# Optimization experiments

Measured on AMD Instinct MI355X. Metric: run time of the kernel, lower is better.

## Reference

```python
import jax, jax.numpy as jnp
import numpy as np

WINDOW = 1024  # sliding-window mask_mod: attend to keys within WINDOW behind the query


def setup_inputs() -> dict:
    key = jax.random.key(0)
    B, L, H, E = 2, 2048, 16, 64
    qkv = jax.random.normal(key, (B, L, 3, H, E), dtype=jnp.float32)
    return {"qkv": qkv}


def reference(qkv) -> jnp.ndarray:
    # Training path of FlexAttention.forward (key_cache/val_cache/cache_seqlens = None).
    B, L, _, H, E = qkv.shape
    q = qkv[:, :, 0]  # [b, l, h, e]
    k = qkv[:, :, 1]
    v = qkv[:, :, 2]

    scale = 1.0 / (E ** 0.5)  # flex_attention default softmax scaling
    scores = jnp.einsum("bqhe,bkhe->bhqk", q, k) * scale  # [b, h, q, kv]

    q_idx = jnp.arange(L)[:, None]
    kv_idx = jnp.arange(L)[None, :]
    dist = q_idx - kv_idx  # [q, kv]

    # score_mod: ALiBi bias, slope_h = 2^(-8*(h+1)/H)
    slopes = jnp.exp2(-8.0 * (jnp.arange(H, dtype=jnp.float32) + 1.0) / H)
    scores = scores - slopes[None, :, None, None] * dist.astype(jnp.float32)

    # and_masks(mask_mod, causal_mask): sliding window AND causal
    mask = (dist >= 0) & (dist < WINDOW)  # causal guarantees >=1 valid key per row
    scores = jnp.where(mask[None, None], scores, -jnp.inf)

    attn = jax.nn.softmax(scores, axis=-1)
    out = jnp.einsum("bhqk,bkhe->bqhe", attn, v)  # [b, l, h, e]
    return out
```

## Files before the change

kernel.cpp:

```cpp
#include <hip/hip_runtime.h>
#include <cstdint>

#define L_SEQ 2048
#define NH 16
#define EDIM 64
#define WINDOW 1024
#define QT 64
#define KT 64
#define LOG2E 1.4426950408889634f
#define M_FIX 16.0f

typedef short bf16x8 __attribute__((ext_vector_type(8)));
typedef short bf16x4 __attribute__((ext_vector_type(4)));
typedef float f32x4 __attribute__((ext_vector_type(4)));

__device__ __forceinline__ short f2bf(float x) {
    uint32_t u = __builtin_bit_cast(uint32_t, x);
    uint32_t r = (u + 0x7fffu + ((u >> 16) & 1u)) >> 16;
    return (short)(r & 0xffffu);
}
__device__ __forceinline__ short f2bf_trunc(float x) {
    return (short)(__builtin_bit_cast(uint32_t, x) >> 16);
}

__device__ __forceinline__ f32x4 mfma16(bf16x4 a, bf16x4 b, f32x4 c) {
#if __has_builtin(__builtin_amdgcn_mfma_f32_16x16x16bf16_1k)
    return __builtin_amdgcn_mfma_f32_16x16x16bf16_1k(a, b, c, 0, 0, 0);
#else
    asm("s_nop 1\n\tv_mfma_f32_16x16x16_bf16 %0, %1, %2, %0"
        : "+v"(c) : "v"(a), "v"(b));
    return c;
#endif
}

__device__ __forceinline__ void async16(const short* g, const short* l) {
    __builtin_amdgcn_global_load_lds(
        (const __attribute__((address_space(1))) void*)(uintptr_t)(g),
        (__attribute__((address_space(3))) void*)(uintptr_t)(l),
        16, 0, 0);
}

__global__ __launch_bounds__(256) void prepass4(const float* __restrict__ qkv,
        short* __restrict__ kw, short* __restrict__ vw) {
    __shared__ float vt[64][68];
    const int x = blockIdx.x;
    const int xcd = x & 7, y = x >> 3;
    const int pairid = xcd * 4 + (y >> 5);
    const int tile = y & 31;
    const int b = pairid >> 4, h = pairid & 15;
    const int tid = threadIdx.x;
    const int tg = pairid * 32 + tile;
    const float* base = qkv + (size_t)b * (L_SEQ * 3072) + (size_t)tile * 64 * 3072 + h * 64;
    short* ko = kw + (size_t)tg * 4096;
    short* vo = vw + (size_t)tg * 4096;

    #pragma unroll
    for (int it = 0; it < 2; ++it) {
        const int c = tid + it * 256;
        const int row = c >> 3, cc = (c & 7) ^ (row & 7);
        const float* src = base + (size_t)row * 3072 + 1024 + cc * 8;
        float4 a = *(const float4*)src, d = *(const float4*)(src + 4);
        short* o = ko + (size_t)c * 8;
        o[0] = f2bf(a.x); o[1] = f2bf(a.y); o[2] = f2bf(a.z); o[3] = f2bf(a.w);
        o[4] = f2bf(d.x); o[5] = f2bf(d.y); o[6] = f2bf(d.z); o[7] = f2bf(d.w);
    }
    {
        const int row = tid >> 2, e0 = (tid & 3) << 4;
        const float* src = base + (size_t)row * 3072 + 2048 + e0;
        #pragma unroll
        for (int q4 = 0; q4 < 4; ++q4) {
            float4 a = *(const float4*)(src + q4 * 4);
            vt[e0 + q4 * 4 + 0][row] = a.x;
            vt[e0 + q4 * 4 + 1][row] = a.y;
            vt[e0 + q4 * 4 + 2][row] = a.z;
            vt[e0 + q4 * 4 + 3][row] = a.w;
        }
    }
    __syncthreads();
    #pragma unroll
    for (int it = 0; it < 2; ++it) {
        const int c = tid + it * 256;
        const int et = c >> 7, a = (c >> 6) & 1, l6 = c & 63;
        const int quad = l6 >> 4, r16 = l6 & 15;
        const int e = et * 16 + r16;
        float4 x0 = *(const float4*)&vt[e][a * 32 + quad * 4];
        float4 x1 = *(const float4*)&vt[e][a * 32 + 16 + quad * 4];
        bf16x8 o8;
        o8[0] = f2bf(x0.x); o8[1] = f2bf(x0.y); o8[2] = f2bf(x0.z); o8[3] = f2bf(x0.w);
        o8[4] = f2bf(x1.x); o8[5] = f2bf(x1.y); o8[6] = f2bf(x1.z); o8[7] = f2bf(x1.w);
        *(bf16x8*)(vo + (size_t)c * 8) = o8;
    }
}

__global__ __launch_bounds__(128, 2) void flexattn_fwd6(
        const float* __restrict__ qkv, const short* __restrict__ kw,
        const short* __restrict__ vw, float* __restrict__ out) {
    __shared__ __align__(16) short kS[2][4096];
    __shared__ __align__(16) short vS[2][4096];

    const int s = blockIdx.y & 31;
    const int k = blockIdx.y >> 5;
    const int t16 = (s + ((k >> 1) << 4)) & 31;
    const int qtile = (k & 1) ? (31 - t16) : t16;
    const int pairid = blockIdx.x * 4 + k;
    const int h = pairid & 15;
    const int b = pairid >> 4;

    const int tid  = threadIdx.x;
    const int w    = tid >> 6;
    const int lane = tid & 63;
    const int quad = lane >> 4;
    const int r16  = lane & 15;
    const int qb   = qtile * QT;
    const int bh32 = (b * NH + h) * 32;
    const int q0   = qb + w * 32 + r16;

    const int t0q = (qb >= WINDOW - 1) ? ((qb - (WINDOW - 1)) >> 6) : 0;
    const int t1  = qtile;
    const int swz = quad ^ (r16 & 7);
    const int cb0 = w * 256;

    {
        const short* ktile = kw + (size_t)(bh32 + t0q) * 4096;
        const short* vtile = vw + (size_t)(bh32 + t0q) * 4096;
        #pragma unroll
        for (int i = 0; i < 4; ++i) {
            const int cb = cb0 + i * 64;
            async16(ktile + (size_t)(cb + lane) * 8, &kS[0][cb * 8]);
            async16(vtile + (size_t)(cb + lane) * 8, &vS[0][cb * 8]);
        }
    }

    const float qscale = 0.125f * LOG2E;
    bf16x8 qfrag[2][2];
    #pragma unroll
    for (int g = 0; g < 2; ++g) {
        const float* qrow = qkv + (size_t)b * (L_SEQ * 3072)
                                + (size_t)(q0 + g * 16) * 3072 + h * 64;
        #pragma unroll
        for (int es = 0; es < 2; ++es) {
            const float* p = qrow + es * 32 + quad * 8;
            float4 a = *(const float4*)p;
            float4 c = *(const float4*)(p + 4);
            bf16x8 f;
            f[0] = f2bf(a.x * qscale); f[1] = f2bf(a.y * qscale);
            f[2] = f2bf(a.z * qscale); f[3] = f2bf(a.w * qscale);
            f[4] = f2bf(c.x * qscale); f[5] = f2bf(c.y * qscale);
            f[6] = f2bf(c.z * qscale); f[7] = f2bf(c.w * qscale);
            qfrag[g][es] = f;
        }
    }

    const float slope2 = __builtin_amdgcn_exp2f(-8.0f * (float)(h + 1) / (float)NH) * LOG2E;
    const float c64 = slope2 * 64.0f;
    f32x4 EA[2][4];
    #pragma unroll
    for (int g = 0; g < 2; ++g)
        #pragma unroll
        for (int ct = 0; ct < 4; ++ct)
            #pragma unroll
            for (int r = 0; r < 4; ++r)
                EA[g][ct][r] = slope2 * (float)(t0q * 64 + ct * 16 + quad * 4 + r
                                                - (q0 + g * 16)) - M_FIX;

    f32x4 O[2][4] = {};
    float rs[2] = {0.f, 0.f};

    for (int kt = t0q; kt <= t1; ++kt) {
        const int cur = (kt - t0q) & 1;
        __syncthreads();
        if (kt < t1) {
            const int nb = cur ^ 1;
            const short* ktile = kw + (size_t)(bh32 + kt + 1) * 4096;
            const short* vtile = vw + (size_t)(bh32 + kt + 1) * 4096;
            #pragma unroll
            for (int i = 0; i < 4; ++i) {
                const int cb = cb0 + i * 64;
                async16(ktile + (size_t)(cb + lane) * 8, &kS[nb][cb * 8]);
                async16(vtile + (size_t)(cb + lane) * 8, &vS[nb][cb * 8]);
            }
        }

        f32x4 S[2][4];
        #pragma unroll
        for (int ct = 0; ct < 4; ++ct) {
            const int c0 = ((ct * 16 + r16) << 3) + swz;
            bf16x8 k0 = *(const bf16x8*)&kS[cur][c0 * 8];
            bf16x8 k1 = *(const bf16x8*)&kS[cur][(c0 ^ 4) * 8];
            #pragma unroll
            for (int g = 0; g < 2; ++g) {
                f32x4 acc = __builtin_amdgcn_mfma_f32_16x16x32_bf16(k0, qfrag[g][0], EA[g][ct], 0, 0, 0);
                S[g][ct]  = __builtin_amdgcn_mfma_f32_16x16x32_bf16(k1, qfrag[g][1], acc, 0, 0, 0);
            }
        }

        bf16x4 pb[2][4];
        if (kt != t0q && kt != t1) {
            #pragma unroll
            for (int g = 0; g < 2; ++g)
                #pragma unroll
                for (int ct = 0; ct < 4; ++ct)
                    #pragma unroll
                    for (int r = 0; r < 4; ++r) {
                        const float pe = __builtin_amdgcn_exp2f(S[g][ct][r]);
                        rs[g] += pe;
                        pb[g][ct][r] = f2bf_trunc(pe);
                    }
        } else {
            const int key0 = kt * 64 + quad * 4;
            #pragma unroll
            for (int g = 0; g < 2; ++g) {
                const int qg = q0 + g * 16;
                #pragma unroll
                for (int ct = 0; ct < 4; ++ct)
                    #pragma unroll
                    for (int r = 0; r < 4; ++r) {
                        const int dist = qg - (key0 + ct * 16 + r);
                        float pe = __builtin_amdgcn_exp2f(S[g][ct][r]);
                        pe = (dist < 0 || dist >= WINDOW) ? 0.0f : pe;
                        rs[g] += pe;
                        pb[g][ct][r] = f2bf_trunc(pe);
                    }
            }
        }

        #pragma unroll
        for (int et = 0; et < 4; ++et) {
            #pragma unroll
            for (int a = 0; a < 2; ++a) {
                bf16x8 v8 = *(const bf16x8*)&vS[cur][(size_t)((et * 2 + a) * 64 + lane) * 8];
                bf16x4 vlo = {v8[0], v8[1], v8[2], v8[3]};
                bf16x4 vhi = {v8[4], v8[5], v8[6], v8[7]};
                #pragma unroll
                for (int g = 0; g < 2; ++g) {
                    O[g][et] = mfma16(vlo, pb[g][a * 2 + 0], O[g][et]);
                    O[g][et] = mfma16(vhi, pb[g][a * 2 + 1], O[g][et]);
                }
            }
        }

        #pragma unroll
        for (int ct = 0; ct < 4; ++ct) {
            EA[0][ct] += c64;
            EA[1][ct] += c64;
        }
    }

    #pragma unroll
    for (int g = 0; g < 2; ++g) {
        float r = rs[g];
        r += __shfl_xor(r, 16, 64);
        r += __shfl_xor(r, 32, 64);
        const float rl = 1.0f / r;
        float* op = out + ((size_t)b * L_SEQ + (q0 + g * 16)) * (NH * EDIM) + h * EDIM;
        #pragma unroll
        for (int et = 0; et < 4; ++et) {
            float4 o4 = {O[g][et][0] * rl, O[g][et][1] * rl,
                         O[g][et][2] * rl, O[g][et][3] * rl};
            *(float4*)(op + et * 16 + quad * 4) = o4;
        }
    }
}

__global__ __launch_bounds__(256, 2) void flexattn_fwd_fb(
        const float* __restrict__ qkv, float* __restrict__ out) {
    __shared__ __align__(16) short kT[KT * 72];
    __shared__ __align__(16) short vB[8 * 64 * 8];
    __shared__ __align__(16) short pT[4][16 * 72];

    const int qtile = blockIdx.x;
    const int h     = blockIdx.y;
    const int b     = blockIdx.z;
    const int tid   = threadIdx.x;
    const int w     = tid >> 6;
    const int lane  = tid & 63;
    const int quad  = lane >> 4;
    const int r16   = lane & 15;
    const int qb = qtile * QT;
    const int rowstride = 3 * NH * EDIM;

    const float* qbase = qkv + ((size_t)b * L_SEQ * 3 + 0) * (NH * EDIM) + h * EDIM;
    const float* kbase = qkv + ((size_t)b * L_SEQ * 3 + 1) * (NH * EDIM) + h * EDIM;
    const float* vbase = qkv + ((size_t)b * L_SEQ * 3 + 2) * (NH * EDIM) + h * EDIM;

    const float qscale = 0.125f * LOG2E;
    bf16x8 qfrag[2];
    {
        const int qg = qb + w * 16 + r16;
        const float* qrow = qbase + (size_t)qg * rowstride;
        #pragma unroll
        for (int es = 0; es < 2; ++es) {
            const float* p = qrow + es * 32 + quad * 8;
            float4 a = *(const float4*)p;
            float4 c = *(const float4*)(p + 4);
            bf16x8 f;
            f[0] = f2bf(a.x * qscale); f[1] = f2bf(a.y * qscale);
            f[2] = f2bf(a.z * qscale); f[3] = f2bf(a.w * qscale);
            f[4] = f2bf(c.x * qscale); f[5] = f2bf(c.y * qscale);
            f[6] = f2bf(c.z * qscale); f[7] = f2bf(c.w * qscale);
            qfrag[es] = f;
        }
    }

    const float slope2 = __builtin_amdgcn_exp2f(-8.0f * (float)(h + 1) / (float)NH) * LOG2E;
    f32x4 O[4] = {{0,0,0,0},{0,0,0,0},{0,0,0,0},{0,0,0,0}};
    float m_run[4] = {-1e30f, -1e30f, -1e30f, -1e30f};
    float l_run[4] = {0.f, 0.f, 0.f, 0.f};

    const int kmin = (qb >= WINDOW - 1) ? (qb - (WINDOW - 1)) : 0;
    const int t0 = kmin >> 6;
    const int t1 = qtile;

    for (int kt = t0; kt <= t1; ++kt) {
        __syncthreads();
        {
            const int j = tid >> 2;
            const int ebase = (tid & 3) * 16;
            const float* krow = kbase + (size_t)(kt * KT + j) * rowstride + ebase;
            const float* vrow = vbase + (size_t)(kt * KT + j) * rowstride + ebase;
            const int js = j >> 5, qd = (j >> 3) & 3, ii = j & 7;
            #pragma unroll
            for (int ee = 0; ee < 4; ++ee) {
                const int e = ebase + ee * 4;
                float4 k4 = *(const float4*)(krow + ee * 4);
                short* kd = &kT[j * 72 + e];
                kd[0] = f2bf(k4.x); kd[1] = f2bf(k4.y);
                kd[2] = f2bf(k4.z); kd[3] = f2bf(k4.w);
                float4 v4 = *(const float4*)(vrow + ee * 4);
                const int et = e >> 4;
                const int ln = qd * 16 + (e & 15);
                short* vd = &vB[(((js * 4 + et) * 64) + ln) * 8 + ii];
                vd[0]  = f2bf(v4.x);
                vd[8]  = f2bf(v4.y);
                vd[16] = f2bf(v4.z);
                vd[24] = f2bf(v4.w);
            }
        }
        __syncthreads();

        f32x4 S[4];
        #pragma unroll
        for (int ct = 0; ct < 4; ++ct) {
            const short* kr = &kT[(ct * 16 + r16) * 72 + quad * 8];
            bf16x8 b0 = *(const bf16x8*)kr;
            bf16x8 b1 = *(const bf16x8*)(kr + 32);
            f32x4 acc = {0.f, 0.f, 0.f, 0.f};
            acc = __builtin_amdgcn_mfma_f32_16x16x32_bf16(qfrag[0], b0, acc, 0, 0, 0);
            acc = __builtin_amdgcn_mfma_f32_16x16x32_bf16(qfrag[1], b1, acc, 0, 0, 0);
            S[ct] = acc;
        }

        const int q0 = qb + w * 16 + quad * 4;
        float p[4][4];
        float mt[4] = {-1e30f, -1e30f, -1e30f, -1e30f};
        #pragma unroll
        for (int ct = 0; ct < 4; ++ct) {
            const int kg = kt * KT + ct * 16 + r16;
            #pragma unroll
            for (int r = 0; r < 4; ++r) {
                const int dist = q0 + r - kg;
                float s2 = S[ct][r] - slope2 * (float)dist;
                if (dist < 0 || dist >= WINDOW) s2 = -1e30f;
                p[ct][r] = s2;
                mt[r] = fmaxf(mt[r], s2);
            }
        }
        #pragma unroll
        for (int d = 1; d < 16; d <<= 1) {
            #pragma unroll
            for (int r = 0; r < 4; ++r)
                mt[r] = fmaxf(mt[r], __shfl_xor(mt[r], d, 64));
        }

        float alpha[4], rsum[4];
        #pragma unroll
        for (int r = 0; r < 4; ++r) {
            const float mn = fmaxf(m_run[r], mt[r]);
            alpha[r] = __builtin_amdgcn_exp2f(m_run[r] - mn);
            m_run[r] = mn;
            float sacc = 0.f;
            #pragma unroll
            for (int ct = 0; ct < 4; ++ct) {
                const float pe = __builtin_amdgcn_exp2f(p[ct][r] - mn);
                p[ct][r] = pe;
                sacc += pe;
            }
            rsum[r] = sacc;
        }
        #pragma unroll
        for (int d = 1; d < 16; d <<= 1) {
            #pragma unroll
            for (int r = 0; r < 4; ++r)
                rsum[r] += __shfl_xor(rsum[r], d, 64);
        }
        #pragma unroll
        for (int r = 0; r < 4; ++r)
            l_run[r] = l_run[r] * alpha[r] + rsum[r];
        #pragma unroll
        for (int et = 0; et < 4; ++et) {
            #pragma unroll
            for (int r = 0; r < 4; ++r)
                O[et][r] *= alpha[r];
        }

        short* pw = &pT[w][0];
        #pragma unroll
        for (int ct = 0; ct < 4; ++ct) {
            #pragma unroll
            for (int r = 0; r < 4; ++r)
                pw[(quad * 4 + r) * 72 + ct * 16 + r16] = f2bf(p[ct][r]);
        }
        bf16x8 aP0 = *(const bf16x8*)(pw + r16 * 72 + quad * 8);
        bf16x8 aP1 = *(const bf16x8*)(pw + r16 * 72 + 32 + quad * 8);

        #pragma unroll
        for (int et = 0; et < 4; ++et) {
            bf16x8 v0 = *(const bf16x8*)(&vB[((0 * 4 + et) * 64 + lane) * 8]);
            O[et] = __builtin_amdgcn_mfma_f32_16x16x32_bf16(aP0, v0, O[et], 0, 0, 0);
            bf16x8 v1 = *(const bf16x8*)(&vB[((1 * 4 + et) * 64 + lane) * 8]);
            O[et] = __builtin_amdgcn_mfma_f32_16x16x32_bf16(aP1, v1, O[et], 0, 0, 0);
        }
    }

    float* obase = out + (((size_t)b * L_SEQ) * NH + (size_t)h) * EDIM;
    #pragma unroll
    for (int r = 0; r < 4; ++r) {
        const int qg = qb + w * 16 + quad * 4 + r;
        const float rl = 1.0f / l_run[r];
        float* orow = obase + (size_t)qg * (NH * EDIM);
        #pragma unroll
        for (int et = 0; et < 4; ++et)
            orow[et * 16 + r16] = O[et][r] * rl;
    }
}

extern "C" void kernel_launch(void* const* d_in, const int* in_sizes, int n_in,
                              void* d_out, int out_size, void* d_ws, size_t ws_size,
                              hipStream_t stream) {
    const float* qkv = (const float*)d_in[0];
    float* out = (float*)d_out;
    const size_t need = (size_t)2 * 1024 * 4096 * sizeof(short);
    if (ws_size >= need) {
        short* kw = (short*)d_ws;
        short* vw = kw + (size_t)1024 * 4096;
        prepass4<<<1024, 256, 0, stream>>>(qkv, kw, vw);
        dim3 grid(8, 128);
        flexattn_fwd6<<<grid, 128, 0, stream>>>(qkv, kw, vw, out);
    } else {
        dim3 gridfb(L_SEQ / QT, NH, 2);
        flexattn_fwd_fb<<<gridfb, 256, 0, stream>>>(qkv, out);
    }
}
```

Baseline: 116.5 us.

## Split key tile across two extra waves per block with LDS reduction

```diff
diff --git a/kernel.cpp b/kernel.cpp
--- a/kernel.cpp
+++ b/kernel.cpp
@@ -92,7 +92,7 @@
     }
 }
 
-__global__ __launch_bounds__(128, 2) void flexattn_fwd6(
+__global__ __launch_bounds__(256, 4) void flexattn_fwd7(
         const float* __restrict__ qkv, const short* __restrict__ kw,
         const short* __restrict__ vw, float* __restrict__ out) {
     __shared__ __align__(16) short kS[2][4096];
@@ -106,25 +106,27 @@
     const int h = pairid & 15;
     const int b = pairid >> 4;
 
-    const int tid  = threadIdx.x;
-    const int w    = tid >> 6;
-    const int lane = tid & 63;
-    const int quad = lane >> 4;
-    const int r16  = lane & 15;
-    const int qb   = qtile * QT;
-    const int bh32 = (b * NH + h) * 32;
-    const int q0   = qb + w * 32 + r16;
+    const int tid   = threadIdx.x;
+    const int w     = tid >> 6;
+    const int lane  = tid & 63;
+    const int quad  = lane >> 4;
+    const int r16   = lane & 15;
+    const int qhalf = w & 1;
+    const int khalf = w >> 1;
+    const int qb    = qtile * QT;
+    const int bh32  = (b * NH + h) * 32;
+    const int q0    = qb + qhalf * 32 + r16;
 
     const int t0q = (qb >= WINDOW - 1) ? ((qb - (WINDOW - 1)) >> 6) : 0;
     const int t1  = qtile;
     const int swz = quad ^ (r16 & 7);
-    const int cb0 = w * 256;
+    const int cb0 = w * 128;
 
     {
         const short* ktile = kw + (size_t)(bh32 + t0q) * 4096;
         const short* vtile = vw + (size_t)(bh32 + t0q) * 4096;
         #pragma unroll
-        for (int i = 0; i < 4; ++i) {
+        for (int i = 0; i < 2; ++i) {
             const int cb = cb0 + i * 64;
             async16(ktile + (size_t)(cb + lane) * 8, &kS[0][cb * 8]);
             async16(vtile + (size_t)(cb + lane) * 8, &vS[0][cb * 8]);
@@ -153,15 +155,15 @@
 
     const float slope2 = __builtin_amdgcn_exp2f(-8.0f * (float)(h + 1) / (float)NH) * LOG2E;
     const float c64 = slope2 * 64.0f;
-    f32x4 EA[2][4];
+    f32x4 EA[2][2];
     #pragma unroll
     for (int g = 0; g < 2; ++g)
         #pragma unroll
-        for (int ct = 0; ct < 4; ++ct)
+        for (int ctl = 0; ctl < 2; ++ctl)
             #pragma unroll
             for (int r = 0; r < 4; ++r)
-                EA[g][ct][r] = slope2 * (float)(t0q * 64 + ct * 16 + quad * 4 + r
-                                                - (q0 + g * 16)) - M_FIX;
+                EA[g][ctl][r] = slope2 * (float)(t0q * 64 + (khalf * 2 + ctl) * 16
+                                                 + quad * 4 + r - (q0 + g * 16)) - M_FIX;
 
     f32x4 O[2][4] = {};
     float rs[2] = {0.f, 0.f};
@@ -174,90 +176,121 @@
             const short* ktile = kw + (size_t)(bh32 + kt + 1) * 4096;
             const short* vtile = vw + (size_t)(bh32 + kt + 1) * 4096;
             #pragma unroll
-            for (int i = 0; i < 4; ++i) {
+            for (int i = 0; i < 2; ++i) {
                 const int cb = cb0 + i * 64;
                 async16(ktile + (size_t)(cb + lane) * 8, &kS[nb][cb * 8]);
                 async16(vtile + (size_t)(cb + lane) * 8, &vS[nb][cb * 8]);
             }
         }
 
-        f32x4 S[2][4];
-        #pragma unroll
-        for (int ct = 0; ct < 4; ++ct) {
+        f32x4 S[2][2];
+        __builtin_amdgcn_s_setprio(1);
+        #pragma unroll
+        for (int ctl = 0; ctl < 2; ++ctl) {
+            const int ct = khalf * 2 + ctl;
             const int c0 = ((ct * 16 + r16) << 3) + swz;
             bf16x8 k0 = *(const bf16x8*)&kS[cur][c0 * 8];
             bf16x8 k1 = *(const bf16x8*)&kS[cur][(c0 ^ 4) * 8];
             #pragma unroll
             for (int g = 0; g < 2; ++g) {
-                f32x4 acc = __builtin_amdgcn_mfma_f32_16x16x32_bf16(k0, qfrag[g][0], EA[g][ct], 0, 0, 0);
-                S[g][ct]  = __builtin_amdgcn_mfma_f32_16x16x32_bf16(k1, qfrag[g][1], acc, 0, 0, 0);
-            }
-        }
-
-        bf16x4 pb[2][4];
+                f32x4 acc = __builtin_amdgcn_mfma_f32_16x16x32_bf16(k0, qfrag[g][0], EA[g][ctl], 0, 0, 0);
+                S[g][ctl] = __builtin_amdgcn_mfma_f32_16x16x32_bf16(k1, qfrag[g][1], acc, 0, 0, 0);
+            }
+        }
+        __builtin_amdgcn_s_setprio(0);
+
+        bf16x4 pb[2][2];
         if (kt != t0q && kt != t1) {
             #pragma unroll
             for (int g = 0; g < 2; ++g)
                 #pragma unroll
-                for (int ct = 0; ct < 4; ++ct)
+                for (int ctl = 0; ctl < 2; ++ctl)
                     #pragma unroll
                     for (int r = 0; r < 4; ++r) {
-                        const float pe = __builtin_amdgcn_exp2f(S[g][ct][r]);
+                        const float pe = __builtin_amdgcn_exp2f(S[g][ctl][r]);
                         rs[g] += pe;
-                        pb[g][ct][r] = f2bf_trunc(pe);
+                        pb[g][ctl][r] = f2bf_trunc(pe);
                     }
         } else {
-            const int key0 = kt * 64 + quad * 4;
+            const int key0 = kt * 64 + khalf * 32 + quad * 4;
             #pragma unroll
             for (int g = 0; g < 2; ++g) {
                 const int qg = q0 + g * 16;
                 #pragma unroll
-                for (int ct = 0; ct < 4; ++ct)
+                for (int ctl = 0; ctl < 2; ++ctl)
                     #pragma unroll
                     for (int r = 0; r < 4; ++r) {
-                        const int dist = qg - (key0 + ct * 16 + r);
-                        float pe = __builtin_amdgcn_exp2f(S[g][ct][r]);
+                        const int dist = qg - (key0 + ctl * 16 + r);
+                        float pe = __builtin_amdgcn_exp2f(S[g][ctl][r]);
                         pe = (dist < 0 || dist >= WINDOW) ? 0.0f : pe;
                         rs[g] += pe;
-                        pb[g][ct][r] = f2bf_trunc(pe);
+                        pb[g][ctl][r] = f2bf_trunc(pe);
                     }
             }
         }
 
+        __builtin_amdgcn_s_setprio(1);
         #pragma unroll
         for (int et = 0; et < 4; ++et) {
-            #pragma unroll
-            for (int a = 0; a < 2; ++a) {
-                bf16x8 v8 = *(const bf16x8*)&vS[cur][(size_t)((et * 2 + a) * 64 + lane) * 8];
-                bf16x4 vlo = {v8[0], v8[1], v8[2], v8[3]};
-                bf16x4 vhi = {v8[4], v8[5], v8[6], v8[7]};
+            bf16x8 v8 = *(const bf16x8*)&vS[cur][(size_t)((et * 2 + khalf) * 64 + lane) * 8];
+            bf16x4 vlo = {v8[0], v8[1], v8[2], v8[3]};
+            bf16x4 vhi = {v8[4], v8[5], v8[6], v8[7]};
+            #pragma unroll
+            for (int g = 0; g < 2; ++g) {
+                O[g][et] = mfma16(vlo, pb[g][0], O[g][et]);
+                O[g][et] = mfma16(vhi, pb[g][1], O[g][et]);
+            }
+        }
+        __builtin_amdgcn_s_setprio(0);
+
+        #pragma unroll
+        for (int ctl = 0; ctl < 2; ++ctl) {
+            EA[0][ctl] += c64;
+            EA[1][ctl] += c64;
+        }
+    }
+
+    __syncthreads();
+    float* oS = (float*)&kS[0][0];
+    float* rS = (float*)&vS[0][0];
+    if (khalf) {
+        float* dst = oS + qhalf * 2048;
+        #pragma unroll
+        for (int g = 0; g < 2; ++g)
+            #pragma unroll
+            for (int et = 0; et < 4; ++et)
                 #pragma unroll
-                for (int g = 0; g < 2; ++g) {
-                    O[g][et] = mfma16(vlo, pb[g][a * 2 + 0], O[g][et]);
-                    O[g][et] = mfma16(vhi, pb[g][a * 2 + 1], O[g][et]);
-                }
-            }
-        }
-
-        #pragma unroll
-        for (int ct = 0; ct < 4; ++ct) {
-            EA[0][ct] += c64;
-            EA[1][ct] += c64;
-        }
-    }
-
-    #pragma unroll
-    for (int g = 0; g < 2; ++g) {
-        float r = rs[g];
-        r += __shfl_xor(r, 16, 64);
-        r += __shfl_xor(r, 32, 64);
-        const float rl = 1.0f / r;
-        float* op = out + ((size_t)b * L_SEQ + (q0 + g * 16)) * (NH * EDIM) + h * EDIM;
-        #pragma unroll
-        for (int et = 0; et < 4; ++et) {
-            float4 o4 = {O[g][et][0] * rl, O[g][et][1] * rl,
-                         O[g][et][2] * rl, O[g][et][3] * rl};
-            *(float4*)(op + et * 16 + quad * 4) = o4;
+                for (int j = 0; j < 4; ++j)
+                    dst[((g * 4 + et) * 4 + j) * 64 + lane] = O[g][et][j];
+        rS[qhalf * 128 + lane]      = rs[0];
+        rS[qhalf * 128 + 64 + lane] = rs[1];
+    }
+    __syncthreads();
+    if (!khalf) {
+        const float* src = oS + qhalf * 2048;
+        #pragma unroll
+        for (int g = 0; g < 2; ++g)
+            #pragma unroll
+            for (int et = 0; et < 4; ++et)
+                #pragma unroll
+                for (int j = 0; j < 4; ++j)
+                    O[g][et][j] += src[((g * 4 + et) * 4 + j) * 64 + lane];
+        rs[0] += rS[qhalf * 128 + lane];
+        rs[1] += rS[qhalf * 128 + 64 + lane];
+
+        #pragma unroll
+        for (int g = 0; g < 2; ++g) {
+            float r = rs[g];
+            r += __shfl_xor(r, 16, 64);
+            r += __shfl_xor(r, 32, 64);
+            const float rl = 1.0f / r;
+            float* op = out + ((size_t)b * L_SEQ + (q0 + g * 16)) * (NH * EDIM) + h * EDIM;
+            #pragma unroll
+            for (int et = 0; et < 4; ++et) {
+                float4 o4 = {O[g][et][0] * rl, O[g][et][1] * rl,
+                             O[g][et][2] * rl, O[g][et][3] * rl};
+                *(float4*)(op + et * 16 + quad * 4) = o4;
+            }
         }
     }
 }
@@ -445,7 +478,7 @@
         short* vw = kw + (size_t)1024 * 4096;
         prepass4<<<1024, 256, 0, stream>>>(qkv, kw, vw);
         dim3 grid(8, 128);
-        flexattn_fwd6<<<grid, 128, 0, stream>>>(qkv, kw, vw, out);
+        flexattn_fwd7<<<grid, 256, 0, stream>>>(qkv, kw, vw, out);
     } else {
         dim3 gridfb(L_SEQ / QT, NH, 2);
         flexattn_fwd_fb<<<gridfb, 256, 0, stream>>>(qkv, out);
```

Result: faster. 112.8 us (-3.2%).

## Replace LDS double-buffering with single-wave blocks loading K/V directly into registers

Applied to the files above, without the earlier changes.

```diff
diff --git a/kernel.cpp b/kernel.cpp
--- a/kernel.cpp
+++ b/kernel.cpp
@@ -31,13 +31,6 @@
         : "+v"(c) : "v"(a), "v"(b));
     return c;
 #endif
-}
-
-__device__ __forceinline__ void async16(const short* g, const short* l) {
-    __builtin_amdgcn_global_load_lds(
-        (const __attribute__((address_space(1))) void*)(uintptr_t)(g),
-        (__attribute__((address_space(3))) void*)(uintptr_t)(l),
-        16, 0, 0);
 }
 
 __global__ __launch_bounds__(256) void prepass4(const float* __restrict__ qkv,
@@ -92,44 +85,32 @@
     }
 }
 
-__global__ __launch_bounds__(128, 2) void flexattn_fwd6(
+__global__ __launch_bounds__(64, 2) void flexattn_fwd12(
         const float* __restrict__ qkv, const short* __restrict__ kw,
         const short* __restrict__ vw, float* __restrict__ out) {
-    __shared__ __align__(16) short kS[2][4096];
-    __shared__ __align__(16) short vS[2][4096];
-
-    const int s = blockIdx.y & 31;
-    const int k = blockIdx.y >> 5;
-    const int t16 = (s + ((k >> 1) << 4)) & 31;
-    const int qtile = (k & 1) ? (31 - t16) : t16;
-    const int pairid = blockIdx.x * 4 + k;
-    const int h = pairid & 15;
-    const int b = pairid >> 4;
-
-    const int tid  = threadIdx.x;
-    const int w    = tid >> 6;
-    const int lane = tid & 63;
+    const int l    = blockIdx.x;
+    const int lane = threadIdx.x;
     const int quad = lane >> 4;
     const int r16  = lane & 15;
-    const int qb   = qtile * QT;
-    const int bh32 = (b * NH + h) * 32;
-    const int q0   = qb + w * 32 + r16;
-
+    const int swz  = quad ^ (r16 & 7);
+
+    const int pairid = (l & 7) * 4 + ((l >> 3) & 3);
+    const int qhalf  = (l >> 5) & 1;
+    const int u      = l >> 6;
+    const int v      = u & 3;
+    const int m      = u >> 2;
+    const int s      = v + ((m >> 2) << 2);
+    const int j      = m & 3;
+    const int qtile  = (j == 0) ? (31 - s) : (j == 1) ? (16 + s)
+                     : (j == 2) ? (15 - s) : s;
+
+    const int h  = pairid & 15;
+    const int b  = pairid >> 4;
+    const int qb = qtile * QT;
+    const int bh32 = pairid * 32;
+    const int q0 = qb + qhalf * 32 + r16;
     const int t0q = (qb >= WINDOW - 1) ? ((qb - (WINDOW - 1)) >> 6) : 0;
     const int t1  = qtile;
-    const int swz = quad ^ (r16 & 7);
-    const int cb0 = w * 256;
-
-    {
-        const short* ktile = kw + (size_t)(bh32 + t0q) * 4096;
-        const short* vtile = vw + (size_t)(bh32 + t0q) * 4096;
-        #pragma unroll
-        for (int i = 0; i < 4; ++i) {
-            const int cb = cb0 + i * 64;
-            async16(ktile + (size_t)(cb + lane) * 8, &kS[0][cb * 8]);
-            async16(vtile + (size_t)(cb + lane) * 8, &vS[0][cb * 8]);
-        }
-    }
 
     const float qscale = 0.125f * LOG2E;
     bf16x8 qfrag[2][2];
@@ -166,85 +147,98 @@
     f32x4 O[2][4] = {};
     float rs[2] = {0.f, 0.f};
 
-    for (int kt = t0q; kt <= t1; ++kt) {
-        const int cur = (kt - t0q) & 1;
-        __syncthreads();
-        if (kt < t1) {
-            const int nb = cur ^ 1;
-            const short* ktile = kw + (size_t)(bh32 + kt + 1) * 4096;
-            const short* vtile = vw + (size_t)(bh32 + kt + 1) * 4096;
-            #pragma unroll
-            for (int i = 0; i < 4; ++i) {
-                const int cb = cb0 + i * 64;
-                async16(ktile + (size_t)(cb + lane) * 8, &kS[nb][cb * 8]);
-                async16(vtile + (size_t)(cb + lane) * 8, &vS[nb][cb * 8]);
-            }
-        }
-
-        f32x4 S[2][4];
-        #pragma unroll
-        for (int ct = 0; ct < 4; ++ct) {
-            const int c0 = ((ct * 16 + r16) << 3) + swz;
-            bf16x8 k0 = *(const bf16x8*)&kS[cur][c0 * 8];
-            bf16x8 k1 = *(const bf16x8*)&kS[cur][(c0 ^ 4) * 8];
-            #pragma unroll
-            for (int g = 0; g < 2; ++g) {
-                f32x4 acc = __builtin_amdgcn_mfma_f32_16x16x32_bf16(k0, qfrag[g][0], EA[g][ct], 0, 0, 0);
-                S[g][ct]  = __builtin_amdgcn_mfma_f32_16x16x32_bf16(k1, qfrag[g][1], acc, 0, 0, 0);
-            }
-        }
-
-        bf16x4 pb[2][4];
-        if (kt != t0q && kt != t1) {
-            #pragma unroll
-            for (int g = 0; g < 2; ++g)
-                #pragma unroll
-                for (int ct = 0; ct < 4; ++ct)
-                    #pragma unroll
-                    for (int r = 0; r < 4; ++r) {
-                        const float pe = __builtin_amdgcn_exp2f(S[g][ct][r]);
-                        rs[g] += pe;
-                        pb[g][ct][r] = f2bf_trunc(pe);
-                    }
-        } else {
-            const int key0 = kt * 64 + quad * 4;
-            #pragma unroll
-            for (int g = 0; g < 2; ++g) {
-                const int qg = q0 + g * 16;
-                #pragma unroll
-                for (int ct = 0; ct < 4; ++ct)
-                    #pragma unroll
-                    for (int r = 0; r < 4; ++r) {
-                        const int dist = qg - (key0 + ct * 16 + r);
-                        float pe = __builtin_amdgcn_exp2f(S[g][ct][r]);
-                        pe = (dist < 0 || dist >= WINDOW) ? 0.0f : pe;
-                        rs[g] += pe;
-                        pb[g][ct][r] = f2bf_trunc(pe);
-                    }
-            }
-        }
-
-        #pragma unroll
-        for (int et = 0; et < 4; ++et) {
-            #pragma unroll
-            for (int a = 0; a < 2; ++a) {
-                bf16x8 v8 = *(const bf16x8*)&vS[cur][(size_t)((et * 2 + a) * 64 + lane) * 8];
-                bf16x4 vlo = {v8[0], v8[1], v8[2], v8[3]};
-                bf16x4 vhi = {v8[4], v8[5], v8[6], v8[7]};
-                #pragma unroll
-                for (int g = 0; g < 2; ++g) {
-                    O[g][et] = mfma16(vlo, pb[g][a * 2 + 0], O[g][et]);
-                    O[g][et] = mfma16(vhi, pb[g][a * 2 + 1], O[g][et]);
-                }
-            }
-        }
-
-        #pragma unroll
-        for (int ct = 0; ct < 4; ++ct) {
-            EA[0][ct] += c64;
-            EA[1][ct] += c64;
-        }
-    }
+#define KLOAD12(DST, TKT) do {                                            \
+        const short* _kp = kw + (size_t)(bh32 + (TKT)) * 4096;            \
+        _Pragma("unroll")                                                 \
+        for (int _ct = 0; _ct < 4; ++_ct) {                               \
+            const int _c0 = ((_ct * 16 + r16) << 3) + swz;                \
+            DST[_ct * 2 + 0] = *(const bf16x8*)(_kp + (size_t)_c0 * 8);   \
+            DST[_ct * 2 + 1] = *(const bf16x8*)(_kp + (size_t)(_c0 ^ 4) * 8); \
+        }                                                                 \
+    } while (0)
+
+#define TILE12(CUR, NXT) do {                                             \
+        bf16x8 vr[8];                                                     \
+        {   const short* _vp = vw + (size_t)(bh32 + kt) * 4096;           \
+            _Pragma("unroll")                                             \
+            for (int _i = 0; _i < 8; ++_i)                                \
+                vr[_i] = *(const bf16x8*)(_vp + (size_t)(_i * 64 + lane) * 8); } \
+        if (kt < t1) KLOAD12(NXT, kt + 1);                                \
+        f32x4 S[2][4];                                                    \
+        __builtin_amdgcn_s_setprio(1);                                    \
+        _Pragma("unroll")                                                 \
+        for (int ct = 0; ct < 4; ++ct) {                                  \
+            _Pragma("unroll")                                             \
+            for (int g = 0; g < 2; ++g) {                                 \
+                f32x4 acc = __builtin_amdgcn_mfma_f32_16x16x32_bf16(      \
+                    CUR[ct * 2 + 0], qfrag[g][0], EA[g][ct], 0, 0, 0);    \
+                S[g][ct] = __builtin_amdgcn_mfma_f32_16x16x32_bf16(       \
+                    CUR[ct * 2 + 1], qfrag[g][1], acc, 0, 0, 0);          \
+            }                                                             \
+        }                                                                 \
+        __builtin_amdgcn_s_setprio(0);                                    \
+        bf16x4 pb[2][4];                                                  \
+        if (kt != t0q && kt != t1) {        \
+            _Pragma("unroll")                                             \
+            for (int g = 0; g < 2; ++g)                                   \
+                _Pragma("unroll")                                         \
+                for (int ct = 0; ct < 4; ++ct)                            \
+                    _Pragma("unroll")                                     \
+                    for (int r = 0; r < 4; ++r) {                         \
+                        const float pe = __builtin_amdgcn_exp2f(S[g][ct][r]); \
+                        rs[g] += pe;                                      \
+                        pb[g][ct][r] = f2bf_trunc(pe);                    \
+                    }                                                     \
+        } else {                          \
+            const int key0 = kt * 64 + quad * 4;                          \
+            _Pragma("unroll")                                             \
+            for (int g = 0; g < 2; ++g) {                                 \
+                const int qg = q0 + g * 16;                               \
+                _Pragma("unroll")                                         \
+                for (int ct = 0; ct < 4; ++ct)                            \
+                    _Pragma("unroll")                                     \
+                    for (int r = 0; r < 4; ++r) {                         \
+                        const int dist = qg - (key0 + ct * 16 + r);       \
+                        float pe = __builtin_amdgcn_exp2f(S[g][ct][r]);   \
+                        pe = (dist < 0 || dist >= WINDOW) ? 0.0f : pe;    \
+                        rs[g] += pe;                                      \
+                        pb[g][ct][r] = f2bf_trunc(pe);                    \
+                    }                                                     \
+            }                                                             \
+        }                                                                 \
+        __builtin_amdgcn_s_setprio(1);                                    \
+        _Pragma("unroll")                                                 \
+        for (int et = 0; et < 4; ++et) {                                  \
+            _Pragma("unroll")                                             \
+            for (int a = 0; a < 2; ++a) {                                 \
+                bf16x8 v8 = vr[et * 2 + a];                               \
+                bf16x4 vlo = {v8[0], v8[1], v8[2], v8[3]};                \
+                bf16x4 vhi = {v8[4], v8[5], v8[6], v8[7]};                \
+                _Pragma("unroll")                                         \
+                for (int g = 0; g < 2; ++g) {                             \
+                    O[g][et] = mfma16(vlo, pb[g][a * 2 + 0], O[g][et]);   \
+                    O[g][et] = mfma16(vhi, pb[g][a * 2 + 1], O[g][et]);   \
+                }                                                         \
+            }                                                             \
+        }                                                                 \
+        __builtin_amdgcn_s_setprio(0);                                    \
+        _Pragma("unroll")                                                 \
+        for (int ct = 0; ct < 4; ++ct) { EA[0][ct] += c64; EA[1][ct] += c64; } \
+    } while (0)
+
+    bf16x8 KA[8], KB[8];
+    KLOAD12(KA, t0q);
+    int kt = t0q;
+    for (;;) {
+        TILE12(KA, KB);
+        if (kt == t1) break;
+        ++kt;
+        TILE12(KB, KA);
+        if (kt == t1) break;
+        ++kt;
+    }
+#undef TILE12
+#undef KLOAD12
 
     #pragma unroll
     for (int g = 0; g < 2; ++g) {
@@ -439,13 +433,13 @@
                               hipStream_t stream) {
     const float* qkv = (const float*)d_in[0];
     float* out = (float*)d_out;
-    const size_t need = (size_t)2 * 1024 * 4096 * sizeof(short);
+    const size_t kv_elems = (size_t)1024 * 4096;
+    const size_t need = 2 * kv_elems * sizeof(short);
     if (ws_size >= need) {
         short* kw = (short*)d_ws;
-        short* vw = kw + (size_t)1024 * 4096;
+        short* vw = kw + kv_elems;
         prepass4<<<1024, 256, 0, stream>>>(qkv, kw, vw);
-        dim3 grid(8, 128);
-        flexattn_fwd6<<<grid, 128, 0, stream>>>(qkv, kw, vw, out);
+        flexattn_fwd12<<<2048, 64, 0, stream>>>(qkv, kw, vw, out);
     } else {
         dim3 gridfb(L_SEQ / QT, NH, 2);
         flexattn_fwd_fb<<<gridfb, 256, 0, stream>>>(qkv, out);
```

Measured after the change: 117.1 us. No clear change (+0.5%).
